# Kernel optimization log

Measured on AMD Instinct MI355X. Metric: run time of the kernel, lower is better.

The kernel has to match this reference:

```python
import jax, jax.numpy as jnp
import numpy as np

B, T, D, DIM = 32, 2048, 1024, 1024


def setup_inputs() -> dict:
    key = jax.random.key(0)
    ks = jax.random.split(key, 7)
    def glorot(k, shape):
        lim = np.sqrt(6.0 / (shape[0] + shape[1]))
        return jax.random.uniform(k, shape, jnp.float32, -lim, lim)
    return {
        "input_states": jax.random.normal(ks[0], (B, T, D), jnp.float32),
        "last_state": jax.random.normal(ks[1], (B, D), jnp.float32),
        "Wy": glorot(ks[2], (D, DIM)),
        "Wh": glorot(ks[3], (D, DIM)),
        "w": glorot(ks[4], (DIM, 1)),
        "Wp": glorot(ks[5], (D, DIM)),
        "Wx": glorot(ks[6], (D, DIM)),
    }


def reference(input_states, last_state, Wy, Wh, w, Wp, Wx):
    # hs: (B,T,dim); last_state projection broadcast over T (the original
    # tiles last_state via a ones-matmul; a plain broadcast is the same math)
    hs = jnp.einsum("btd,de->bte", input_states, Wy)
    hproj = last_state @ Wh                      # (B,dim)
    m = jax.nn.relu(hs + hproj[:, None, :])      # (B,T,dim)
    scores = jnp.einsum("bte,eo->bt", m, w[:, :1])  # squeeze last dim
    alpha = jax.nn.softmax(scores, axis=-1)      # (B,T)
    r = jnp.einsum("bt,btd->bd", alpha, input_states)
    out = jax.nn.relu(r @ Wp + last_state @ Wx)  # (B,dim)
    return out
```

## Files before the change

### kernel.cpp

```cpp
#include <hip/hip_runtime.h>
#include <hip/hip_bf16.h>
#include <stdint.h>

#define BB 32
#define TT 2048
#define DD 1024
#define DIMQ 1024
#define MTOT (BB*TT)

typedef __attribute__((ext_vector_type(8))) __bf16 bf16x8;
typedef __attribute__((ext_vector_type(4))) float f32x4;

__device__ __forceinline__ unsigned short f2bf(float f) {
    unsigned int u = __float_as_uint(f);
    u += 0x7FFF + ((u >> 16) & 1);
    return (unsigned short)(u >> 16);
}
__device__ __forceinline__ float bf2f(unsigned short s) {
    return __uint_as_float(((unsigned int)s) << 16);
}

__device__ __forceinline__ void load_lds16(const void* g, void* l) {
    __builtin_amdgcn_global_load_lds(
        (const __attribute__((address_space(1))) unsigned int*)g,
        (__attribute__((address_space(3))) unsigned int*)l,
        16, 0, 0);
}

__global__ void cast_x(const float* __restrict__ x, unsigned short* __restrict__ xb) {
    long i = ((long)blockIdx.x * blockDim.x + threadIdx.x) * 8;
    float4 a = *(const float4*)(x + i);
    float4 b = *(const float4*)(x + i + 4);
    uint4 o;
    o.x = (unsigned int)f2bf(a.x) | ((unsigned int)f2bf(a.y) << 16);
    o.y = (unsigned int)f2bf(a.z) | ((unsigned int)f2bf(a.w) << 16);
    o.z = (unsigned int)f2bf(b.x) | ((unsigned int)f2bf(b.y) << 16);
    o.w = (unsigned int)f2bf(b.z) | ((unsigned int)f2bf(b.w) << 16);
    *(uint4*)(xb + i) = o;
}

__global__ void transpose_cast(const float* __restrict__ Wsrc, unsigned short* __restrict__ Wdst) {
    __shared__ float tile[32][33];
    int bx = blockIdx.x * 32;
    int by = blockIdx.y * 32;
    int tx = threadIdx.x & 31;
    int ty4 = (threadIdx.x >> 5) * 4;
    #pragma unroll
    for (int r = 0; r < 4; r++)
        tile[ty4 + r][tx] = Wsrc[(size_t)(by + ty4 + r) * DIMQ + bx + tx];
    __syncthreads();
    #pragma unroll
    for (int r = 0; r < 4; r++)
        Wdst[(size_t)(bx + ty4 + r) * DD + by + tx] = f2bf(tile[tx][ty4 + r]);
}

__global__ void vecmat2(const float* __restrict__ last,
                        const float* __restrict__ Wh, const float* __restrict__ Wx,
                        float* __restrict__ hproj, float* __restrict__ lsWx) {
    __shared__ float vs[DD];
    __shared__ float red[4][64];
    int b = blockIdx.y;
    int e0 = blockIdx.x * 64;
    const float* Mat = blockIdx.z ? Wx : Wh;
    float* outp = blockIdx.z ? lsWx : hproj;
    int tid = threadIdx.x;
    for (int d = tid; d < DD; d += 256) vs[d] = last[b * DD + d];
    __syncthreads();
    int e = tid & 63, dg = tid >> 6;
    int d0 = dg * 256;
    const float* Mp = Mat + (size_t)d0 * DIMQ + e0 + e;
    float acc = 0.f;
    #pragma unroll 8
    for (int d = 0; d < 256; d++) acc += vs[d0 + d] * Mp[(size_t)d * DIMQ];
    red[dg][e] = acc;
    __syncthreads();
    if (dg == 0)
        outp[b * DIMQ + e0 + e] = red[0][e] + red[1][e] + red[2][e] + red[3][e];
}

__global__ void gemm_scores(const unsigned short* __restrict__ Xb,
                            const unsigned short* __restrict__ WyT,
                            const float* __restrict__ hproj,
                            const float* __restrict__ wvec,
                            float* __restrict__ partials) {
    __shared__ unsigned short Alds[4096];
    __shared__ unsigned short Blds[4096];
    __shared__ float lp[128];

    int x = blockIdx.x;
    int mtile = x >> 3, ntile = x & 7;
    int tid = threadIdx.x;
    int lane = tid & 63;
    int wave = tid >> 6;

    if (tid < 128) lp[tid] = 0.f;

    const int rowA0 = mtile * 128;
    const int colB0 = ntile * 128;

    int sub0 = tid >> 6,          ln0 = tid & 63;
    int r0 = sub0 * 16 + (ln0 & 15), ko0 = (ln0 >> 4) << 3;
    int sub1 = (tid + 256) >> 6,  ln1 = (tid + 256) & 63;
    int r1 = sub1 * 16 + (ln1 & 15), ko1 = (ln1 >> 4) << 3;

    const unsigned short* Ag0 = Xb  + (size_t)(rowA0 + r0) * DD + ko0;
    const unsigned short* Ag1 = Xb  + (size_t)(rowA0 + r1) * DD + ko1;
    const unsigned short* Bg0 = WyT + (size_t)(colB0 + r0) * DD + ko0;
    const unsigned short* Bg1 = WyT + (size_t)(colB0 + r1) * DD + ko1;

    unsigned short* Al0 = &Alds[tid * 8];
    unsigned short* Al1 = &Alds[(tid + 256) * 8];
    unsigned short* Bl0 = &Blds[tid * 8];
    unsigned short* Bl1 = &Blds[(tid + 256) * 8];

    int wm = (wave >> 1) * 4;
    int wn = (wave & 1) * 4;

    f32x4 acc[4][4] = {};

    for (int kk = 0; kk < DD; kk += 32) {
        load_lds16(Ag0 + kk, Al0);
        load_lds16(Ag1 + kk, Al1);
        load_lds16(Bg0 + kk, Bl0);
        load_lds16(Bg1 + kk, Bl1);
        __syncthreads();

        bf16x8 af[4], bfr[4];
        #pragma unroll
        for (int i = 0; i < 4; i++)
            af[i] = *reinterpret_cast<const bf16x8*>(&Alds[((wm + i) * 64 + lane) * 8]);
        #pragma unroll
        for (int j = 0; j < 4; j++)
            bfr[j] = *reinterpret_cast<const bf16x8*>(&Blds[((wn + j) * 64 + lane) * 8]);
        #pragma unroll
        for (int i = 0; i < 4; i++)
            #pragma unroll
            for (int j = 0; j < 4; j++)
                acc[i][j] = __builtin_amdgcn_mfma_f32_16x16x32_bf16(af[i], bfr[j], acc[i][j], 0, 0, 0);
        __syncthreads();
    }

    int b = rowA0 / TT;
    int q = lane >> 4, l15 = lane & 15;
    int wmRow = (wave >> 1) * 64, wnCol = (wave & 1) * 64;

    float hpv[4], wvv[4];
    #pragma unroll
    for (int j = 0; j < 4; j++) {
        int n = wnCol + j * 16 + l15;
        hpv[j] = hproj[b * DIMQ + colB0 + n];
        wvv[j] = wvec[colB0 + n];
    }

    #pragma unroll
    for (int i = 0; i < 4; i++) {
        f32x4 s = {0.f, 0.f, 0.f, 0.f};
        #pragma unroll
        for (int j = 0; j < 4; j++) {
            #pragma unroll
            for (int r = 0; r < 4; r++) {
                float v = acc[i][j][r] + hpv[j];
                v = v > 0.f ? v : 0.f;
                s[r] += v * wvv[j];
            }
        }
        #pragma unroll
        for (int off = 1; off < 16; off <<= 1) {
            s[0] += __shfl_xor(s[0], off);
            s[1] += __shfl_xor(s[1], off);
            s[2] += __shfl_xor(s[2], off);
            s[3] += __shfl_xor(s[3], off);
        }
        if (l15 == 0) {
            int mrow = wmRow + i * 16 + q * 4;
            atomicAdd(&lp[mrow + 0], s[0]);
            atomicAdd(&lp[mrow + 1], s[1]);
            atomicAdd(&lp[mrow + 2], s[2]);
            atomicAdd(&lp[mrow + 3], s[3]);
        }
    }
    __syncthreads();
    if (tid < 128)
        partials[(size_t)ntile * MTOT + rowA0 + tid] = lp[tid];
}

__global__ void sum_partials(const float* __restrict__ partials, float* __restrict__ scores) {
    int i0 = (blockIdx.x * 256 + threadIdx.x) * 4;
    float4 v = {0.f, 0.f, 0.f, 0.f};
    #pragma unroll
    for (int p = 0; p < 8; p++) {
        float4 t = *(const float4*)(partials + (size_t)p * MTOT + i0);
        v.x += t.x; v.y += t.y; v.z += t.z; v.w += t.w;
    }
    *(float4*)(scores + i0) = v;
}

__global__ void softmax_alpha(const float* __restrict__ scores, float* __restrict__ alpha) {
    __shared__ float wred[4];
    __shared__ float wsum[4];
    int b = blockIdx.x;
    int tid = threadIdx.x;
    float s[8];
    float mx = -1e30f;
    #pragma unroll
    for (int c = 0; c < 8; c++) {
        float v = scores[b * TT + tid + c * 256];
        s[c] = v;
        mx = fmaxf(mx, v);
    }
    for (int off = 32; off; off >>= 1) mx = fmaxf(mx, __shfl_xor(mx, off));
    if ((tid & 63) == 0) wred[tid >> 6] = mx;
    __syncthreads();
    mx = fmaxf(fmaxf(wred[0], wred[1]), fmaxf(wred[2], wred[3]));
    float sum = 0.f;
    #pragma unroll
    for (int c = 0; c < 8; c++) { s[c] = expf(s[c] - mx); sum += s[c]; }
    for (int off = 32; off; off >>= 1) sum += __shfl_xor(sum, off);
    if ((tid & 63) == 0) wsum[tid >> 6] = sum;
    __syncthreads();
    sum = wsum[0] + wsum[1] + wsum[2] + wsum[3];
    float inv = 1.f / sum;
    #pragma unroll
    for (int c = 0; c < 8; c++) alpha[b * TT + tid + c * 256] = s[c] * inv;
}

__global__ void weighted_sum(const unsigned short* __restrict__ Xb,
                             const float* __restrict__ alpha,
                             float* __restrict__ r_part) {
    __shared__ float al[128];
    int tc = blockIdx.x, b = blockIdx.y, tid = threadIdx.x;
    if (tid < 128) al[tid] = alpha[b * TT + tc * 128 + tid];
    __syncthreads();
    int d0 = tid * 4;
    const unsigned short* base = Xb + ((size_t)(b * TT + tc * 128)) * DD + d0;
    f32x4 acc = {0.f, 0.f, 0.f, 0.f};
    #pragma unroll 2
    for (int t = 0; t < 128; t++) {
        ushort4 xv = *(const ushort4*)(base + (size_t)t * DD);
        float a_ = al[t];
        acc[0] += a_ * bf2f(xv.x);
        acc[1] += a_ * bf2f(xv.y);
        acc[2] += a_ * bf2f(xv.z);
        acc[3] += a_ * bf2f(xv.w);
    }
    float* o = r_part + ((size_t)tc * BB + b) * DD + d0;
    *(float4*)o = *(float4*)&acc;
}

__global__ void reduce_r(const float* __restrict__ r_part, float* __restrict__ rbuf) {
    int b = blockIdx.x, tid = threadIdx.x;
    int d0 = tid * 4;
    float4 v = {0.f, 0.f, 0.f, 0.f};
    #pragma unroll
    for (int p = 0; p < 16; p++) {
        float4 t = *(const float4*)(r_part + ((size_t)p * BB + b) * DD + d0);
        v.x += t.x; v.y += t.y; v.z += t.z; v.w += t.w;
    }
    *(float4*)(rbuf + b * DD + d0) = v;
}

__global__ void final_out(const float* __restrict__ rbuf, const float* __restrict__ Wp,
                          const float* __restrict__ lsWx, float* __restrict__ out) {
    __shared__ float rs[DD];
    __shared__ float red[4][64];
    int b = blockIdx.y;
    int e0 = blockIdx.x * 64;
    int tid = threadIdx.x;
    for (int d = tid; d < DD; d += 256) rs[d] = rbuf[b * DD + d];
    __syncthreads();
    int e = tid & 63, dg = tid >> 6;
    int d0 = dg * 256;
    const float* Mp = Wp + (size_t)d0 * DIMQ + e0 + e;
    float acc = 0.f;
    #pragma unroll 8
    for (int d = 0; d < 256; d++) acc += rs[d0 + d] * Mp[(size_t)d * DIMQ];
    red[dg][e] = acc;
    __syncthreads();
    if (dg == 0) {
        float v = red[0][e] + red[1][e] + red[2][e] + red[3][e]
                + lsWx[b * DIMQ + e0 + e];
        out[b * DIMQ + e0 + e] = fmaxf(v, 0.f);
    }
}

extern "C" void kernel_launch(void* const* d_in, const int* in_sizes, int n_in,
                              void* d_out, int out_size, void* d_ws, size_t ws_size,
                              hipStream_t stream) {
    const float* x    = (const float*)d_in[0];
    const float* last = (const float*)d_in[1];
    const float* Wy   = (const float*)d_in[2];
    const float* Wh   = (const float*)d_in[3];
    const float* w    = (const float*)d_in[4];
    const float* Wp   = (const float*)d_in[5];
    const float* Wx   = (const float*)d_in[6];
    float* out = (float*)d_out;

    char* ws = (char*)d_ws;
    unsigned short* Xb   = (unsigned short*)(ws);
    unsigned short* WyT  = (unsigned short*)(ws + 134217728);
    float* hproj         = (float*)(ws + 136314880);
    float* lsWx          = (float*)(ws + 136445952);
    float* partials      = (float*)(ws + 136577024);
    float* scores        = (float*)(ws + 138674176);
    float* alpha         = (float*)(ws + 138936320);
    float* r_part        = (float*)(ws + 139198464);
    float* rbuf          = (float*)(ws + 141295616);

    cast_x<<<(BB*TT*DD/8 + 255) / 256, 256, 0, stream>>>(x, Xb);
    transpose_cast<<<dim3(32, 32), 256, 0, stream>>>(Wy, WyT);
    vecmat2<<<dim3(DIMQ/64, BB, 2), 256, 0, stream>>>(last, Wh, Wx, hproj, lsWx);
    gemm_scores<<<512 * 8, 256, 0, stream>>>(Xb, WyT, hproj, w, partials);
    sum_partials<<<MTOT/(256*4), 256, 0, stream>>>(partials, scores);
    softmax_alpha<<<BB, 256, 0, stream>>>(scores, alpha);
    weighted_sum<<<dim3(TT/128, BB), 256, 0, stream>>>(Xb, alpha, r_part);
    reduce_r<<<BB, 256, 0, stream>>>(r_part, rbuf);
    final_out<<<dim3(DIMQ/64, BB), 256, 0, stream>>>(rbuf, Wp, lsWx, out);
}
```

Measured before the change: 698.7 us.

## Widen GEMM tile to 128x256 and fold partial reductions into consumers

The scores GEMM tile grows from 128x128 to 128x256 (each wave computes 64x128), which halves the N-tiles and so halves the number of times the large bf16 input matrix is re-read from memory. The sum_partials and reduce_r kernels are removed, and their reductions are folded into softmax_alpha and final_out, saving two launches and their intermediate buffers. cast_x now handles 4 elements per thread instead of 8. The larger accumulator array (128 floats per lane) raises register pressure and may lower occupancy, even with launch_bounds(256,2).

```diff
diff --git a/kernel.cpp b/kernel.cpp
--- a/kernel.cpp
+++ b/kernel.cpp
@@ -28,15 +28,11 @@
 }
 
 __global__ void cast_x(const float* __restrict__ x, unsigned short* __restrict__ xb) {
-    long i = ((long)blockIdx.x * blockDim.x + threadIdx.x) * 8;
+    long i = ((long)blockIdx.x * blockDim.x + threadIdx.x) * 4;
     float4 a = *(const float4*)(x + i);
-    float4 b = *(const float4*)(x + i + 4);
-    uint4 o;
-    o.x = (unsigned int)f2bf(a.x) | ((unsigned int)f2bf(a.y) << 16);
-    o.y = (unsigned int)f2bf(a.z) | ((unsigned int)f2bf(a.w) << 16);
-    o.z = (unsigned int)f2bf(b.x) | ((unsigned int)f2bf(b.y) << 16);
-    o.w = (unsigned int)f2bf(b.z) | ((unsigned int)f2bf(b.w) << 16);
-    *(uint4*)(xb + i) = o;
+    ushort4 o;
+    o.x = f2bf(a.x); o.y = f2bf(a.y); o.z = f2bf(a.z); o.w = f2bf(a.w);
+    *(ushort4*)(xb + i) = o;
 }
 
 __global__ void transpose_cast(const float* __restrict__ Wsrc, unsigned short* __restrict__ Wdst) {
@@ -78,17 +74,18 @@
         outp[b * DIMQ + e0 + e] = red[0][e] + red[1][e] + red[2][e] + red[3][e];
 }
 
-__global__ void gemm_scores(const unsigned short* __restrict__ Xb,
-                            const unsigned short* __restrict__ WyT,
-                            const float* __restrict__ hproj,
-                            const float* __restrict__ wvec,
-                            float* __restrict__ partials) {
+__global__ __launch_bounds__(256, 2)
+void gemm_scores(const unsigned short* __restrict__ Xb,
+                 const unsigned short* __restrict__ WyT,
+                 const float* __restrict__ hproj,
+                 const float* __restrict__ wvec,
+                 float* __restrict__ partials) {
     __shared__ unsigned short Alds[4096];
-    __shared__ unsigned short Blds[4096];
+    __shared__ unsigned short Blds[8192];
     __shared__ float lp[128];
 
     int x = blockIdx.x;
-    int mtile = x >> 3, ntile = x & 7;
+    int mtile = x >> 2, ntile = x & 3;
     int tid = threadIdx.x;
     int lane = tid & 63;
     int wave = tid >> 6;
@@ -96,67 +93,71 @@
     if (tid < 128) lp[tid] = 0.f;
 
     const int rowA0 = mtile * 128;
-    const int colB0 = ntile * 128;
-
-    int sub0 = tid >> 6,          ln0 = tid & 63;
-    int r0 = sub0 * 16 + (ln0 & 15), ko0 = (ln0 >> 4) << 3;
-    int sub1 = (tid + 256) >> 6,  ln1 = (tid + 256) & 63;
-    int r1 = sub1 * 16 + (ln1 & 15), ko1 = (ln1 >> 4) << 3;
-
-    const unsigned short* Ag0 = Xb  + (size_t)(rowA0 + r0) * DD + ko0;
-    const unsigned short* Ag1 = Xb  + (size_t)(rowA0 + r1) * DD + ko1;
-    const unsigned short* Bg0 = WyT + (size_t)(colB0 + r0) * DD + ko0;
-    const unsigned short* Bg1 = WyT + (size_t)(colB0 + r1) * DD + ko1;
+    const int colB0 = ntile * 256;
+
+    int rsel = lane & 15;
+    int koff = (lane >> 4) * 8;
+    int s0 = tid >> 6;
+
+    const unsigned short* Ag0 = Xb  + (size_t)(rowA0 + s0 * 16 + rsel) * DD + koff;
+    const unsigned short* Ag1 = Ag0 + (size_t)64 * DD;
+    const unsigned short* Bg0 = WyT + (size_t)(colB0 + s0 * 16 + rsel) * DD + koff;
+    const unsigned short* Bg1 = Bg0 + (size_t)64 * DD;
+    const unsigned short* Bg2 = Bg0 + (size_t)128 * DD;
+    const unsigned short* Bg3 = Bg0 + (size_t)192 * DD;
 
     unsigned short* Al0 = &Alds[tid * 8];
     unsigned short* Al1 = &Alds[(tid + 256) * 8];
     unsigned short* Bl0 = &Blds[tid * 8];
     unsigned short* Bl1 = &Blds[(tid + 256) * 8];
-
-    int wm = (wave >> 1) * 4;
-    int wn = (wave & 1) * 4;
-
-    f32x4 acc[4][4] = {};
+    unsigned short* Bl2 = &Blds[(tid + 512) * 8];
+    unsigned short* Bl3 = &Blds[(tid + 768) * 8];
+
+    int wr = wave >> 1;
+    int wc = wave & 1;
+
+    f32x4 acc[4][8] = {};
 
     for (int kk = 0; kk < DD; kk += 32) {
         load_lds16(Ag0 + kk, Al0);
         load_lds16(Ag1 + kk, Al1);
         load_lds16(Bg0 + kk, Bl0);
         load_lds16(Bg1 + kk, Bl1);
+        load_lds16(Bg2 + kk, Bl2);
+        load_lds16(Bg3 + kk, Bl3);
         __syncthreads();
 
-        bf16x8 af[4], bfr[4];
+        bf16x8 af[4], bfr[8];
         #pragma unroll
         for (int i = 0; i < 4; i++)
-            af[i] = *reinterpret_cast<const bf16x8*>(&Alds[((wm + i) * 64 + lane) * 8]);
-        #pragma unroll
-        for (int j = 0; j < 4; j++)
-            bfr[j] = *reinterpret_cast<const bf16x8*>(&Blds[((wn + j) * 64 + lane) * 8]);
+            af[i] = *reinterpret_cast<const bf16x8*>(&Alds[((wr * 4 + i) * 64 + lane) * 8]);
+        #pragma unroll
+        for (int j = 0; j < 8; j++)
+            bfr[j] = *reinterpret_cast<const bf16x8*>(&Blds[((wc * 8 + j) * 64 + lane) * 8]);
         #pragma unroll
         for (int i = 0; i < 4; i++)
             #pragma unroll
-            for (int j = 0; j < 4; j++)
+            for (int j = 0; j < 8; j++)
                 acc[i][j] = __builtin_amdgcn_mfma_f32_16x16x32_bf16(af[i], bfr[j], acc[i][j], 0, 0, 0);
         __syncthreads();
     }
 
     int b = rowA0 / TT;
     int q = lane >> 4, l15 = lane & 15;
-    int wmRow = (wave >> 1) * 64, wnCol = (wave & 1) * 64;
-
-    float hpv[4], wvv[4];
-    #pragma unroll
-    for (int j = 0; j < 4; j++) {
-        int n = wnCol + j * 16 + l15;
-        hpv[j] = hproj[b * DIMQ + colB0 + n];
-        wvv[j] = wvec[colB0 + n];
+
+    float hpv[8], wvv[8];
+    #pragma unroll
+    for (int j = 0; j < 8; j++) {
+        int n = colB0 + wc * 128 + j * 16 + l15;
+        hpv[j] = hproj[b * DIMQ + n];
+        wvv[j] = wvec[n];
     }
 
     #pragma unroll
     for (int i = 0; i < 4; i++) {
         f32x4 s = {0.f, 0.f, 0.f, 0.f};
         #pragma unroll
-        for (int j = 0; j < 4; j++) {
+        for (int j = 0; j < 8; j++) {
             #pragma unroll
             for (int r = 0; r < 4; r++) {
                 float v = acc[i][j][r] + hpv[j];
@@ -172,7 +173,7 @@
             s[3] += __shfl_xor(s[3], off);
         }
         if (l15 == 0) {
-            int mrow = wmRow + i * 16 + q * 4;
+            int mrow = wr * 64 + i * 16 + q * 4;
             atomicAdd(&lp[mrow + 0], s[0]);
             atomicAdd(&lp[mrow + 1], s[1]);
             atomicAdd(&lp[mrow + 2], s[2]);
@@ -184,18 +185,7 @@
         partials[(size_t)ntile * MTOT + rowA0 + tid] = lp[tid];
 }
 
-__global__ void sum_partials(const float* __restrict__ partials, float* __restrict__ scores) {
-    int i0 = (blockIdx.x * 256 + threadIdx.x) * 4;
-    float4 v = {0.f, 0.f, 0.f, 0.f};
-    #pragma unroll
-    for (int p = 0; p < 8; p++) {
-        float4 t = *(const float4*)(partials + (size_t)p * MTOT + i0);
-        v.x += t.x; v.y += t.y; v.z += t.z; v.w += t.w;
-    }
-    *(float4*)(scores + i0) = v;
-}
-
-__global__ void softmax_alpha(const float* __restrict__ scores, float* __restrict__ alpha) {
+__global__ void softmax_alpha(const float* __restrict__ partials, float* __restrict__ alpha) {
     __shared__ float wred[4];
     __shared__ float wsum[4];
     int b = blockIdx.x;
@@ -204,7 +194,10 @@
     float mx = -1e30f;
     #pragma unroll
     for (int c = 0; c < 8; c++) {
-        float v = scores[b * TT + tid + c * 256];
+        int t = b * TT + tid + c * 256;
+        float v = 0.f;
+        #pragma unroll
+        for (int p = 0; p < 4; p++) v += partials[(size_t)p * MTOT + t];
         s[c] = v;
         mx = fmaxf(mx, v);
     }
@@ -247,26 +240,19 @@
     *(float4*)o = *(float4*)&acc;
 }
 
-__global__ void reduce_r(const float* __restrict__ r_part, float* __restrict__ rbuf) {
-    int b = blockIdx.x, tid = threadIdx.x;
-    int d0 = tid * 4;
-    float4 v = {0.f, 0.f, 0.f, 0.f};
-    #pragma unroll
-    for (int p = 0; p < 16; p++) {
-        float4 t = *(const float4*)(r_part + ((size_t)p * BB + b) * DD + d0);
-        v.x += t.x; v.y += t.y; v.z += t.z; v.w += t.w;
-    }
-    *(float4*)(rbuf + b * DD + d0) = v;
-}
-
-__global__ void final_out(const float* __restrict__ rbuf, const float* __restrict__ Wp,
+__global__ void final_out(const float* __restrict__ r_part, const float* __restrict__ Wp,
                           const float* __restrict__ lsWx, float* __restrict__ out) {
     __shared__ float rs[DD];
     __shared__ float red[4][64];
     int b = blockIdx.y;
     int e0 = blockIdx.x * 64;
     int tid = threadIdx.x;
-    for (int d = tid; d < DD; d += 256) rs[d] = rbuf[b * DD + d];
+    for (int d = tid; d < DD; d += 256) {
+        float v = 0.f;
+        #pragma unroll
+        for (int p = 0; p < 16; p++) v += r_part[((size_t)p * BB + b) * DD + d];
+        rs[d] = v;
+    }
     __syncthreads();
     int e = tid & 63, dg = tid >> 6;
     int d0 = dg * 256;
@@ -301,18 +287,14 @@
     float* hproj         = (float*)(ws + 136314880);
     float* lsWx          = (float*)(ws + 136445952);
     float* partials      = (float*)(ws + 136577024);
-    float* scores        = (float*)(ws + 138674176);
-    float* alpha         = (float*)(ws + 138936320);
-    float* r_part        = (float*)(ws + 139198464);
-    float* rbuf          = (float*)(ws + 141295616);
-
-    cast_x<<<(BB*TT*DD/8 + 255) / 256, 256, 0, stream>>>(x, Xb);
+    float* alpha         = (float*)(ws + 137625600);
+    float* r_part        = (float*)(ws + 137887744);
+
+    cast_x<<<BB*TT*DD/4/256, 256, 0, stream>>>(x, Xb);
     transpose_cast<<<dim3(32, 32), 256, 0, stream>>>(Wy, WyT);
     vecmat2<<<dim3(DIMQ/64, BB, 2), 256, 0, stream>>>(last, Wh, Wx, hproj, lsWx);
-    gemm_scores<<<512 * 8, 256, 0, stream>>>(Xb, WyT, hproj, w, partials);
-    sum_partials<<<MTOT/(256*4), 256, 0, stream>>>(partials, scores);
-    softmax_alpha<<<BB, 256, 0, stream>>>(scores, alpha);
+    gemm_scores<<<512 * 4, 256, 0, stream>>>(Xb, WyT, hproj, w, partials);
+    softmax_alpha<<<BB, 256, 0, stream>>>(partials, alpha);
     weighted_sum<<<dim3(TT/128, BB), 256, 0, stream>>>(Xb, alpha, r_part);
-    reduce_r<<<BB, 256, 0, stream>>>(r_part, rbuf);
-    final_out<<<dim3(DIMQ/64, BB), 256, 0, stream>>>(rbuf, Wp, lsWx, out);
-}
+    final_out<<<dim3(DIMQ/64, BB), 256, 0, stream>>>(r_part, Wp, lsWx, out);
+}
```

After: 643.6 us. 7.9% less time.
